# Kernel tuning notes

Hardware: AMD Instinct MI355X
Metric: run time of the kernel (lower is better)

Reference implementation:

```python
import jax, jax.numpy as jnp
import numpy as np

N_NODES = 100000
N_EDGES = 1600000
T = 64          # num_timesteps (graphs)
D_IN = 256
D_H = 256
D_OUT = 16


def setup_inputs() -> dict:
    key = jax.random.key(0)
    ks = jax.random.split(key, 10)
    s = 1.0 / np.sqrt(D_H)
    x = jax.random.normal(ks[0], (N_NODES, D_IN), dtype=jnp.float32)
    edge_index = jax.random.randint(ks[1], (2, N_EDGES), 0, N_NODES, dtype=jnp.int64)
    ptr = (jnp.arange(T + 1, dtype=jnp.int64) * (N_NODES // T))  # even split of nodes into T snapshots
    return {
        "x": x,
        "edge_index": edge_index,
        "ptr": ptr,
        "W1": jax.random.normal(ks[2], (D_IN, D_H), dtype=jnp.float32) * s,
        "b1": jnp.zeros((D_H,), dtype=jnp.float32),
        "W2": jax.random.normal(ks[3], (D_H, D_H), dtype=jnp.float32) * s,
        "b2": jnp.zeros((D_H,), dtype=jnp.float32),
        "w_ih": jax.random.normal(ks[4], (3 * D_H, D_H), dtype=jnp.float32) * s,
        "w_hh": jax.random.normal(ks[5], (3 * D_H, D_H), dtype=jnp.float32) * s,
        "b_ih": jnp.zeros((3 * D_H,), dtype=jnp.float32),
        "b_hh": jnp.zeros((3 * D_H,), dtype=jnp.float32),
        "Wc": jax.random.normal(ks[6], (D_OUT, D_H), dtype=jnp.float32) * s,
        "bc": jnp.zeros((D_OUT,), dtype=jnp.float32),
    }


def _gcn_conv(x, W, b, src, dst, deg_inv_sqrt):
    # PyG GCNConv with self-loops: out_i = sum_j 1/sqrt(d_i d_j) * (x_j W) + (1/d_i) x_i W + b
    xw = x @ W                                            # [N, H]
    coef = deg_inv_sqrt[src] * deg_inv_sqrt[dst]          # [E]
    msg = xw[src] * coef[:, None]                         # [E, H] gather-scale
    agg = jax.ops.segment_sum(msg, dst, num_segments=N_NODES)
    return agg + xw * (deg_inv_sqrt ** 2)[:, None] + b


def _gru_final(seq, w_ih, w_hh, b_ih, b_hh):
    # torch nn.GRU, 1 layer, gate order (r, z, n). seq: [T, H] (batch=1)
    def step(h, x):
        gx = x @ w_ih.T + b_ih
        gh = h @ w_hh.T + b_hh
        xr, xz, xn = jnp.split(gx, 3)
        hr, hz, hn = jnp.split(gh, 3)
        r = jax.nn.sigmoid(xr + hr)
        z = jax.nn.sigmoid(xz + hz)
        n = jnp.tanh(xn + r * hn)
        h_new = (1.0 - z) * n + z * h
        return h_new, None
    h0 = jnp.zeros((D_H,), dtype=seq.dtype)
    h_final, _ = jax.lax.scan(step, h0, seq)
    return h_final


def reference(x, edge_index, ptr, W1, b1, W2, b2, w_ih, w_hh, b_ih, b_hh, Wc, bc):
    src, dst = edge_index[0], edge_index[1]
    # degree with self-loops
    deg = jax.ops.segment_sum(jnp.ones_like(dst, dtype=x.dtype), dst, num_segments=N_NODES) + 1.0
    deg_inv_sqrt = jax.lax.rsqrt(deg)

    h = jax.nn.relu(_gcn_conv(x, W1, b1, src, dst, deg_inv_sqrt))
    h = jax.nn.relu(_gcn_conv(h, W2, b2, src, dst, deg_inv_sqrt))

    # global_mean_pool over timestep segments derived from ptr
    seg = jnp.searchsorted(ptr, jnp.arange(N_NODES), side="right") - 1      # [N]
    sums = jax.ops.segment_sum(h, seg, num_segments=T)                       # [T, H]
    counts = (ptr[1:] - ptr[:-1]).astype(h.dtype)                            # [T]
    h_pooled = sums / jnp.maximum(counts, 1.0)[:, None]

    h_final = _gru_final(h_pooled, w_ih, w_hh, b_ih, b_hh)                   # [H]
    out = h_final @ Wc.T + bc                                                # [D_OUT]
    return out[None, :]                                                     # [1, D_OUT]
```

## Files before the change

kernel.cpp:

```cpp
#include <hip/hip_runtime.h>
#include <hip/hip_bf16.h>
#include <math.h>


static inline size_t align512(size_t x){ return (x + 511) & ~size_t(511); }

typedef _Float16 h2_t __attribute__((ext_vector_type(2)));
typedef unsigned short ushort_t;
typedef short bf16x8 __attribute__((ext_vector_type(8)));
typedef float f32x4 __attribute__((ext_vector_type(4)));
typedef float f32x2 __attribute__((ext_vector_type(2)));

#if defined(__has_builtin)
#if __has_builtin(__builtin_amdgcn_fdot2)
#define HAS_FDOT2 1
#endif
#if __has_builtin(__builtin_amdgcn_cvt_pk_f32_fp8) && __has_builtin(__builtin_amdgcn_cvt_pk_fp8_f32)
#define HAS_FP8CVT 1
#endif
#endif

__device__ inline ushort_t f2bf(float f){
  unsigned u = __float_as_uint(f);
  unsigned r = u + 0x7FFFu + ((u >> 16) & 1u);
  return (ushort_t)(r >> 16);
}
__device__ inline float bf2f(ushort_t h){ return __uint_as_float(((unsigned)h) << 16); }
__device__ inline unsigned pk2bf(float lo, float hi){
  return ((unsigned)f2bf(hi) << 16) | (unsigned)f2bf(lo);
}
__device__ inline bf16x8 as_bf16x8(uint4 u){
  union { uint4 u4; bf16x8 b; } c; c.u4 = u; return c.b;
}


__device__ inline unsigned char f2fp8(float x){
#ifdef HAS_FP8CVT
  int p = __builtin_amdgcn_cvt_pk_fp8_f32(x, x, 0, false);
  return (unsigned char)(p & 0xFF);
#else
  unsigned u = __float_as_uint(x);
  unsigned s = (u >> 24) & 0x80u;
  unsigned um = u & 0x7FFFFFFFu;
  if (um >= 0x43E00000u) return (unsigned char)(s | 0x7E);
  if (um <  0x3C000000u) return (unsigned char)s;
  unsigned r = um + 0x7FFFFu + ((um >> 20) & 1u);
  unsigned e = (r >> 23) & 0xFF, m = (r >> 20) & 7u;
  return (unsigned char)(s | ((e - 120u) << 3) | m);
#endif
}
__device__ inline void fp8x4_to_f32(unsigned v, float& a, float& b, float& c, float& d){
#ifdef HAS_FP8CVT
  f32x2 lo = __builtin_amdgcn_cvt_pk_f32_fp8(v, false);
  f32x2 hi = __builtin_amdgcn_cvt_pk_f32_fp8(v, true);
  a = lo.x; b = lo.y; c = hi.x; d = hi.y;
#else
  auto d1 = [](unsigned char t)->float{
    unsigned s = (t >> 7) & 1u, e = (t >> 3) & 0xFu, m = t & 7u;
    float v = (e == 0) ? ldexpf((float)m, -9) : ldexpf(8.0f + (float)m, (int)e - 10);
    return s ? -v : v;
  };
  a = d1(v & 0xFF); b = d1((v >> 8) & 0xFF); c = d1((v >> 16) & 0xFF); d = d1(v >> 24);
#endif
}


__global__ void count_kernel(const int* __restrict__ ei, int* __restrict__ cnt, int E){
  int e = blockIdx.x*256 + threadIdx.x;
  if (e < E) atomicAdd(&cnt[ei[E + e]], 1);
}

__global__ void dis_kernel(const int* __restrict__ cnt, float* __restrict__ dis, int N){
  int i = blockIdx.x*256 + threadIdx.x;
  if (i < N) dis[i] = rsqrtf((float)cnt[i] + 1.0f);
}

__global__ void scan_block_kernel(const int* __restrict__ cnt, int* __restrict__ rp,
                                  int* __restrict__ bsum, int N){
  __shared__ int s[2][1024];
  int t = threadIdx.x; int i = blockIdx.x*1024 + t;
  int v = (i < N) ? cnt[i] : 0;
  int cur = 0; s[0][t] = v; __syncthreads();
  for (int off = 1; off < 1024; off <<= 1){
    int nxt = cur ^ 1;
    int val = s[cur][t];
    if (t >= off) val += s[cur][t - off];
    s[nxt][t] = val; cur = nxt; __syncthreads();
  }
  if (i < N) rp[i+1] = s[cur][t];
  if (t == 1023) bsum[blockIdx.x] = s[cur][1023];
}

__global__ void scan_sums_kernel(int* __restrict__ bsum, int nb){
  __shared__ int s[128];
  int t = threadIdx.x;
  if (t < nb) s[t] = bsum[t];
  __syncthreads();
  if (t == 0){ int acc = 0; for (int b = 0; b < nb; b++){ int v = s[b]; s[b] = acc; acc += v; } }
  __syncthreads();
  if (t < nb) bsum[t] = s[t];
}

__global__ void add_off_kernel(int* __restrict__ rp, const int* __restrict__ bsum,
                               int* __restrict__ cnt, int N){
  int i = blockIdx.x*256 + threadIdx.x;
  if (i < N){ rp[i+1] += bsum[i >> 10]; cnt[i] = 0; }
  if (i == 0) rp[0] = 0;
}

__global__ void fill_kernel(const int* __restrict__ ei, const int* __restrict__ rp,
                            int* __restrict__ cnt, int* __restrict__ csrc, int E){
  int e = blockIdx.x*256 + threadIdx.x;
  if (e < E){
    int s = ei[e]; int d = ei[E + e];
    int pos = rp[d] + atomicAdd(&cnt[d], 1);
    csrc[pos] = s;
  }
}


__global__ void packW_kernel(const float* __restrict__ W, uint4* __restrict__ Wp){
  int idx = blockIdx.x*256 + threadIdx.x;
  int lane = idx & 63;
  int blk  = idx >> 6;
  int q    = blk & 7;
  int t16  = blk >> 3;
  int n = t16*16 + (lane & 15);
  int k = q*32 + (lane >> 4)*8;
  uint4 v;
  v.x = pk2bf(W[(size_t)(k+0)*256 + n], W[(size_t)(k+1)*256 + n]);
  v.y = pk2bf(W[(size_t)(k+2)*256 + n], W[(size_t)(k+3)*256 + n]);
  v.z = pk2bf(W[(size_t)(k+4)*256 + n], W[(size_t)(k+5)*256 + n]);
  v.w = pk2bf(W[(size_t)(k+6)*256 + n], W[(size_t)(k+7)*256 + n]);
  Wp[idx] = v;
}


template<bool A_BF16>
__global__ __launch_bounds__(256, 2) void gemm_mfma(const void* __restrict__ Ap,
                                                    const uint4* __restrict__ Wp,
                                                    unsigned char* __restrict__ out, int N){
  __shared__ __align__(16) ushort_t As[2][128][40];
  int tid  = threadIdx.x;
  int lane = tid & 63;
  int wave = tid >> 6;
  int wr = wave >> 1, wc = wave & 1;
  int quad = lane >> 4;
  int l15  = lane & 15;
  int r0 = blockIdx.x * 128;
  int cb = blockIdx.y;

  uint4 bfr[4][8];
  {
    const uint4* wpb = Wp + (size_t)(cb*2 + wc) * 2048;
    #pragma unroll
    for (int ct = 0; ct < 4; ct++)
      #pragma unroll
      for (int q = 0; q < 8; q++)
        bfr[ct][q] = wpb[(ct*8 + q)*64 + lane];
  }

  f32x4 acc[4][4];
  #pragma unroll
  for (int rt = 0; rt < 4; rt++)
    #pragma unroll
    for (int ct = 0; ct < 4; ct++)
      acc[rt][ct] = f32x4{0.f, 0.f, 0.f, 0.f};

  int srow = tid >> 1;
  int shalf = tid & 1;
  int grow = min(r0 + srow, N - 1);

  auto load_stage = [&](int it, uint4& v0, uint4& v1){
    int k0 = it*32 + shalf*16;
    if constexpr (A_BF16){
      const ushort_t* Ab = (const ushort_t*)Ap;
      const uint4* ga = (const uint4*)(Ab + (size_t)grow*256 + k0);
      v0 = ga[0]; v1 = ga[1];
    } else {
      const float* Af = (const float*)Ap;
      const float4* ga = (const float4*)(Af + (size_t)grow*256 + k0);
      float4 f0 = ga[0], f1 = ga[1], f2 = ga[2], f3 = ga[3];
      v0.x = pk2bf(f0.x, f0.y); v0.y = pk2bf(f0.z, f0.w);
      v0.z = pk2bf(f1.x, f1.y); v0.w = pk2bf(f1.z, f1.w);
      v1.x = pk2bf(f2.x, f2.y); v1.y = pk2bf(f2.z, f2.w);
      v1.z = pk2bf(f3.x, f3.y); v1.w = pk2bf(f3.z, f3.w);
    }
  };
  auto write_stage = [&](int b, uint4 v0, uint4 v1){
    *(uint4*)&As[b][srow][shalf*16]     = v0;
    *(uint4*)&As[b][srow][shalf*16 + 8] = v1;
  };

  {
    uint4 v0, v1;
    load_stage(0, v0, v1);
    write_stage(0, v0, v1);
  }
  __syncthreads();

  #pragma unroll
  for (int it = 0; it < 8; it++){
    const int b = it & 1;
    uint4 n0, n1;
    if (it < 7) load_stage(it + 1, n0, n1);
    #pragma unroll
    for (int rt = 0; rt < 4; rt++){
      int arow = wr*64 + rt*16 + l15;
      uint4 av = *(const uint4*)&As[b][arow][quad*8];
      bf16x8 af = as_bf16x8(av);
      #pragma unroll
      for (int ct = 0; ct < 4; ct++)
        acc[rt][ct] = __builtin_amdgcn_mfma_f32_16x16x32_bf16(
            af, as_bf16x8(bfr[ct][it]), acc[rt][ct], 0, 0, 0);
    }
    if (it < 7){
      write_stage(b ^ 1, n0, n1);
      __syncthreads();
    }
  }

  int crow0 = r0 + wr*64 + quad*4;
  int ccol0 = cb*128 + wc*64 + l15;
  #pragma unroll
  for (int rt = 0; rt < 4; rt++){
    #pragma unroll
    for (int g = 0; g < 4; g++){
      int row = crow0 + rt*16 + g;
      if (row < N){
        #pragma unroll
        for (int ct = 0; ct < 4; ct++)
          out[(size_t)row*256 + ccol0 + ct*16] = f2fp8(acc[rt][ct][g]);
      }
    }
  }
}


__global__ __launch_bounds__(256) void agg_kernel(const unsigned char* __restrict__ xw,
                                                  const float* __restrict__ dis,
                                                  const int* __restrict__ rp,
                                                  const int* __restrict__ csrc,
                                                  const float* __restrict__ bias,
                                                  ushort_t* __restrict__ out, int N){
  int node = blockIdx.x*8 + (threadIdx.x >> 5);
  int lane = threadIdx.x & 31;
  if (node >= N) return;
  const uint2* xw2 = (const uint2*)xw;
  float di = dis[node];
  float sc = di * di;
  float acc[8];
  {
    uint2 a = xw2[(size_t)node*32 + lane];
    float v0,v1,v2,v3,v4,v5,v6,v7;
    fp8x4_to_f32(a.x, v0, v1, v2, v3);
    fp8x4_to_f32(a.y, v4, v5, v6, v7);
    acc[0]=v0*sc; acc[1]=v1*sc; acc[2]=v2*sc; acc[3]=v3*sc;
    acc[4]=v4*sc; acc[5]=v5*sc; acc[6]=v6*sc; acc[7]=v7*sc;
  }
  int e0 = rp[node], e1 = rp[node+1];
  for (int e = e0; e < e1; e++){
    int s = csrc[e];
    float cc = dis[s] * di;
    uint2 v = xw2[(size_t)s*32 + lane];
    float v0,v1,v2,v3,v4,v5,v6,v7;
    fp8x4_to_f32(v.x, v0, v1, v2, v3);
    fp8x4_to_f32(v.y, v4, v5, v6, v7);
    acc[0] = fmaf(v0, cc, acc[0]);
    acc[1] = fmaf(v1, cc, acc[1]);
    acc[2] = fmaf(v2, cc, acc[2]);
    acc[3] = fmaf(v3, cc, acc[3]);
    acc[4] = fmaf(v4, cc, acc[4]);
    acc[5] = fmaf(v5, cc, acc[5]);
    acc[6] = fmaf(v6, cc, acc[6]);
    acc[7] = fmaf(v7, cc, acc[7]);
  }
  const float4* b4 = (const float4*)bias;
  float4 bA = b4[lane*2], bB = b4[lane*2+1];
  acc[0] = fmaxf(acc[0] + bA.x, 0.f);
  acc[1] = fmaxf(acc[1] + bA.y, 0.f);
  acc[2] = fmaxf(acc[2] + bA.z, 0.f);
  acc[3] = fmaxf(acc[3] + bA.w, 0.f);
  acc[4] = fmaxf(acc[4] + bB.x, 0.f);
  acc[5] = fmaxf(acc[5] + bB.y, 0.f);
  acc[6] = fmaxf(acc[6] + bB.z, 0.f);
  acc[7] = fmaxf(acc[7] + bB.w, 0.f);
  uint4 o;
  o.x = pk2bf(acc[0], acc[1]);
  o.y = pk2bf(acc[2], acc[3]);
  o.z = pk2bf(acc[4], acc[5]);
  o.w = pk2bf(acc[6], acc[7]);
  ((uint4*)out)[(size_t)node*32 + lane] = o;
}


__global__ void pool_kernel(const ushort_t* __restrict__ h, const int* __restrict__ ptr,
                            float* __restrict__ hp){
  int t = blockIdx.x; int part = blockIdx.y; int c = threadIdx.x;
  int s0 = ptr[t], s1 = ptr[t+1];
  int len = s1 - s0;
  int chunk = (len + 7) / 8;
  int r0 = s0 + part*chunk;
  int r1 = min(r0 + chunk, s1);
  float acc = 0.f;
  for (int r = r0; r < r1; r++) acc += bf2f(h[(size_t)r*256 + c]);
  if (r1 > r0) atomicAdd(&hp[t*256 + c], acc);
}

__global__ void hp_div_kernel(float* __restrict__ hp, const int* __restrict__ ptr){
  int t = blockIdx.x; int c = threadIdx.x;
  float cf = (float)max(ptr[t+1] - ptr[t], 1);
  hp[t*256 + c] /= cf;
}


__global__ __launch_bounds__(768) void gx_kernel(const float* __restrict__ hp,
                                                 const float* __restrict__ wih,
                                                 const float* __restrict__ bih,
                                                 float* __restrict__ gx){
  __shared__ float xs[256];
  int t = blockIdx.x; int g = threadIdx.x;
  if (g < 256) xs[g] = hp[t*256 + g];
  __syncthreads();
  float acc = bih[g];
  const float* wr = wih + (size_t)g*256;
  #pragma unroll 4
  for (int k = 0; k < 256; k++) acc = fmaf(xs[k], wr[k], acc);
  gx[t*768 + g] = acc;
}


__global__ __launch_bounds__(512, 2) void gru_kernel(const float* __restrict__ gx,
                                                     const float* __restrict__ whh,
                                                     const float* __restrict__ bhh,
                                                     const float* __restrict__ Wc,
                                                     const float* __restrict__ bc,
                                                     float* __restrict__ out){
  __shared__ _Float16 hh[256];
  __shared__ float hfin[256];
  int tid = threadIdx.x;
  int i = tid >> 1;
  int half = tid & 1;

  h2_t wr[64], wz[64], wn[64];
  {
    const float2* w2 = (const float2*)whh;
    size_t base = (size_t)half * 64;
    const float2* pr = w2 + (size_t)i*128       + base;
    const float2* pz = w2 + (size_t)(i+256)*128 + base;
    const float2* pn = w2 + (size_t)(i+512)*128 + base;
    #pragma unroll
    for (int k = 0; k < 64; k++){
      float2 a = pr[k];
      float2 b = pz[k];
      float2 c = pn[k];
      wr[k] = h2_t{(_Float16)a.x, (_Float16)a.y};
      wz[k] = h2_t{(_Float16)b.x, (_Float16)b.y};
      wn[k] = h2_t{(_Float16)c.x, (_Float16)c.y};
    }
  }
  float bR = bhh[i], bZ = bhh[i+256], bN = bhh[i+512];
  float h = 0.f;

  for (int t = 0; t < 64; t++){
    if (half == 0) hh[i] = (_Float16)h;
    __syncthreads();
    float gxr = gx[t*768 + i];
    float gxz = gx[t*768 + 256 + i];
    float gxn = gx[t*768 + 512 + i];
    const h2_t* hp2 = ((const h2_t*)hh) + half*64;
    float accR = 0.f, accZ = 0.f, accN = 0.f;
    #pragma unroll
    for (int k = 0; k < 64; k++){
      h2_t hv = hp2[k];
#ifdef HAS_FDOT2
      accR = __builtin_amdgcn_fdot2(hv, wr[k], accR, false);
      accZ = __builtin_amdgcn_fdot2(hv, wz[k], accZ, false);
      accN = __builtin_amdgcn_fdot2(hv, wn[k], accN, false);
#else
      accR = fmaf((float)hv.x, (float)wr[k].x, accR);
      accR = fmaf((float)hv.y, (float)wr[k].y, accR);
      accZ = fmaf((float)hv.x, (float)wz[k].x, accZ);
      accZ = fmaf((float)hv.y, (float)wz[k].y, accZ);
      accN = fmaf((float)hv.x, (float)wn[k].x, accN);
      accN = fmaf((float)hv.y, (float)wn[k].y, accN);
#endif
    }
    accR += __shfl_xor(accR, 1);
    accZ += __shfl_xor(accZ, 1);
    accN += __shfl_xor(accN, 1);
    float r = 1.f/(1.f + expf(-(gxr + accR + bR)));
    float z = 1.f/(1.f + expf(-(gxz + accZ + bZ)));
    float n = tanhf(gxn + r*(accN + bN));
    float hnew = (1.f - z)*n + z*h;
    __syncthreads();
    h = hnew;
  }

  if (half == 0) hfin[i] = h;
  __syncthreads();
  if (tid < 16){
    float acc = bc[tid];
    const float* wrow = Wc + (size_t)tid*256;
    for (int k = 0; k < 256; k++) acc = fmaf(hfin[k], wrow[k], acc);
    out[tid] = acc;
  }
}

extern "C" void kernel_launch(void* const* d_in, const int* in_sizes, int n_in,
                              void* d_out, int out_size, void* d_ws, size_t ws_size,
                              hipStream_t stream){
  const float* x   = (const float*)d_in[0];
  const int*   ei  = (const int*)d_in[1];
  const int*   ptr = (const int*)d_in[2];
  const float* W1  = (const float*)d_in[3];
  const float* b1  = (const float*)d_in[4];
  const float* W2  = (const float*)d_in[5];
  const float* b2  = (const float*)d_in[6];
  const float* wih = (const float*)d_in[7];
  const float* whh = (const float*)d_in[8];
  const float* bih = (const float*)d_in[9];
  const float* bhh = (const float*)d_in[10];
  const float* Wc  = (const float*)d_in[11];
  const float* bc  = (const float*)d_in[12];
  float* outp = (float*)d_out;

  const int N = in_sizes[0] / 256;
  const int E = in_sizes[1] / 2;

  char* w = (char*)d_ws;
  size_t off = 0;
  auto alloc = [&](size_t bytes){ void* p = w + off; off = align512(off + bytes); return p; };
  unsigned char* bufA = (unsigned char*)alloc((size_t)N*256);
  ushort_t*      bufB = (ushort_t*)alloc((size_t)N*256*2);
  float* dis  = (float*)alloc((size_t)N*4);
  int*   cnt  = (int*)  alloc((size_t)N*4);
  int*   rp   = (int*)  alloc((size_t)(N+1)*4);
  int*   bsum = (int*)  alloc(128*4);
  int*   csrc = (int*)  alloc((size_t)E*4);
  uint4* Wp1  = (uint4*)alloc(8192*16);
  uint4* Wp2  = (uint4*)alloc(8192*16);
  float* hp   = (float*)alloc((size_t)64*256*4);
  float* gxb  = (float*)alloc((size_t)64*768*4);
  (void)ws_size; (void)n_in; (void)out_size;

  hipMemsetAsync(cnt, 0, (size_t)N*4, stream);
  hipMemsetAsync(hp,  0, (size_t)64*256*4, stream);

  count_kernel<<<(E+255)/256, 256, 0, stream>>>(ei, cnt, E);
  dis_kernel<<<(N+255)/256, 256, 0, stream>>>(cnt, dis, N);
  int nb = (N + 1023) / 1024;
  scan_block_kernel<<<nb, 1024, 0, stream>>>(cnt, rp, bsum, N);
  scan_sums_kernel<<<1, 128, 0, stream>>>(bsum, nb);
  add_off_kernel<<<(N+255)/256, 256, 0, stream>>>(rp, bsum, cnt, N);
  fill_kernel<<<(E+255)/256, 256, 0, stream>>>(ei, rp, cnt, csrc, E);
  packW_kernel<<<32, 256, 0, stream>>>(W1, Wp1);
  packW_kernel<<<32, 256, 0, stream>>>(W2, Wp2);

  gemm_mfma<false><<<dim3((N+127)/128, 2), 256, 0, stream>>>(x, Wp1, bufA, N);
  agg_kernel<<<(N+7)/8, 256, 0, stream>>>(bufA, dis, rp, csrc, b1, bufB, N);
  gemm_mfma<true><<<dim3((N+127)/128, 2), 256, 0, stream>>>(bufB, Wp2, bufA, N);
  agg_kernel<<<(N+7)/8, 256, 0, stream>>>(bufA, dis, rp, csrc, b2, bufB, N);

  pool_kernel<<<dim3(64, 8), 256, 0, stream>>>(bufB, ptr, hp);
  hp_div_kernel<<<64, 256, 0, stream>>>(hp, ptr);
  gx_kernel<<<64, 768, 0, stream>>>(hp, wih, bih, gxb);
  gru_kernel<<<1, 512, 0, stream>>>(gxb, whh, bhh, Wc, bc, outp);
}
```

Baseline: 816.0 us.

## Store GEMM output in column-sliced layout and aggregate per slice with precomputed coefficients

The GEMM now writes its fp8 output as 8 slices of 32 columns, each a contiguous [N,32] array. The aggregation kernel runs one grid dimension per slice, so each slice's gather working set (about 3.2MB) can stay resident in cache instead of gathering full 256-byte rows at random. Edge coefficients dis[s]*dis[d] are computed once in fill_kernel and stored as fp16 in CSR order, which removes the dis[s] gather in both aggregation passes. In exchange, the CSR index and coefficient arrays are read 8 times per pass, there are 8x more threads each doing narrower work, and coefficient precision drops to fp16.

Measured after the change: 1.002 ms. +22.8%, slower.

```diff
diff --git a/kernel.cpp b/kernel.cpp
--- a/kernel.cpp
+++ b/kernel.cpp
@@ -109,12 +109,15 @@
 }
 
 __global__ void fill_kernel(const int* __restrict__ ei, const int* __restrict__ rp,
-                            int* __restrict__ cnt, int* __restrict__ csrc, int E){
+                            int* __restrict__ cnt, int* __restrict__ csrc,
+                            const float* __restrict__ dis, _Float16* __restrict__ coef,
+                            int E){
   int e = blockIdx.x*256 + threadIdx.x;
   if (e < E){
     int s = ei[e]; int d = ei[E + e];
     int pos = rp[d] + atomicAdd(&cnt[d], 1);
     csrc[pos] = s;
+    coef[pos] = (_Float16)(dis[s] * dis[d]);
   }
 }
 
@@ -229,68 +232,59 @@
       int row = crow0 + rt*16 + g;
       if (row < N){
         #pragma unroll
-        for (int ct = 0; ct < 4; ct++)
-          out[(size_t)row*256 + ccol0 + ct*16] = f2fp8(acc[rt][ct][g]);
+        for (int ct = 0; ct < 4; ct++){
+          int col = ccol0 + ct*16;
+          out[((size_t)(col >> 5)*N + row)*32 + (col & 31)] = f2fp8(acc[rt][ct][g]);
+        }
       }
     }
   }
 }
 
 
-__global__ __launch_bounds__(256) void agg_kernel(const unsigned char* __restrict__ xw,
-                                                  const float* __restrict__ dis,
-                                                  const int* __restrict__ rp,
-                                                  const int* __restrict__ csrc,
-                                                  const float* __restrict__ bias,
-                                                  ushort_t* __restrict__ out, int N){
-  int node = blockIdx.x*8 + (threadIdx.x >> 5);
-  int lane = threadIdx.x & 31;
+__global__ __launch_bounds__(256) void agg_slice(const unsigned char* __restrict__ xw,
+                                                 const float* __restrict__ dis,
+                                                 const int* __restrict__ rp,
+                                                 const int* __restrict__ csrc,
+                                                 const _Float16* __restrict__ coef,
+                                                 const float* __restrict__ bias,
+                                                 ushort_t* __restrict__ out, int N){
+  int slice = blockIdx.x;
+  int node  = blockIdx.y*32 + (threadIdx.x >> 3);
+  int lane8 = threadIdx.x & 7;
   if (node >= N) return;
-  const uint2* xw2 = (const uint2*)xw;
+  const unsigned* xwp = (const unsigned*)xw;
+  size_t sbase = (size_t)slice * N;
   float di = dis[node];
-  float sc = di * di;
-  float acc[8];
+  float acc0, acc1, acc2, acc3;
   {
-    uint2 a = xw2[(size_t)node*32 + lane];
-    float v0,v1,v2,v3,v4,v5,v6,v7;
-    fp8x4_to_f32(a.x, v0, v1, v2, v3);
-    fp8x4_to_f32(a.y, v4, v5, v6, v7);
-    acc[0]=v0*sc; acc[1]=v1*sc; acc[2]=v2*sc; acc[3]=v3*sc;
-    acc[4]=v4*sc; acc[5]=v5*sc; acc[6]=v6*sc; acc[7]=v7*sc;
+    unsigned a = xwp[(sbase + node)*8 + lane8];
+    float v0,v1,v2,v3;
+    fp8x4_to_f32(a, v0, v1, v2, v3);
+    float sc = di * di;
+    acc0 = v0*sc; acc1 = v1*sc; acc2 = v2*sc; acc3 = v3*sc;
   }
   int e0 = rp[node], e1 = rp[node+1];
   for (int e = e0; e < e1; e++){
     int s = csrc[e];
-    float cc = dis[s] * di;
-    uint2 v = xw2[(size_t)s*32 + lane];
-    float v0,v1,v2,v3,v4,v5,v6,v7;
-    fp8x4_to_f32(v.x, v0, v1, v2, v3);
-    fp8x4_to_f32(v.y, v4, v5, v6, v7);
-    acc[0] = fmaf(v0, cc, acc[0]);
-    acc[1] = fmaf(v1, cc, acc[1]);
-    acc[2] = fmaf(v2, cc, acc[2]);
-    acc[3] = fmaf(v3, cc, acc[3]);
-    acc[4] = fmaf(v4, cc, acc[4]);
-    acc[5] = fmaf(v5, cc, acc[5]);
-    acc[6] = fmaf(v6, cc, acc[6]);
-    acc[7] = fmaf(v7, cc, acc[7]);
-  }
-  const float4* b4 = (const float4*)bias;
-  float4 bA = b4[lane*2], bB = b4[lane*2+1];
-  acc[0] = fmaxf(acc[0] + bA.x, 0.f);
-  acc[1] = fmaxf(acc[1] + bA.y, 0.f);
-  acc[2] = fmaxf(acc[2] + bA.z, 0.f);
-  acc[3] = fmaxf(acc[3] + bA.w, 0.f);
-  acc[4] = fmaxf(acc[4] + bB.x, 0.f);
-  acc[5] = fmaxf(acc[5] + bB.y, 0.f);
-  acc[6] = fmaxf(acc[6] + bB.z, 0.f);
-  acc[7] = fmaxf(acc[7] + bB.w, 0.f);
-  uint4 o;
-  o.x = pk2bf(acc[0], acc[1]);
-  o.y = pk2bf(acc[2], acc[3]);
-  o.z = pk2bf(acc[4], acc[5]);
-  o.w = pk2bf(acc[6], acc[7]);
-  ((uint4*)out)[(size_t)node*32 + lane] = o;
+    float cc = (float)coef[e];
+    unsigned v = xwp[(sbase + s)*8 + lane8];
+    float v0,v1,v2,v3;
+    fp8x4_to_f32(v, v0, v1, v2, v3);
+    acc0 = fmaf(v0, cc, acc0);
+    acc1 = fmaf(v1, cc, acc1);
+    acc2 = fmaf(v2, cc, acc2);
+    acc3 = fmaf(v3, cc, acc3);
+  }
+  float4 b = ((const float4*)bias)[slice*8 + lane8];
+  acc0 = fmaxf(acc0 + b.x, 0.f);
+  acc1 = fmaxf(acc1 + b.y, 0.f);
+  acc2 = fmaxf(acc2 + b.z, 0.f);
+  acc3 = fmaxf(acc3 + b.w, 0.f);
+  uint2 o;
+  o.x = pk2bf(acc0, acc1);
+  o.y = pk2bf(acc2, acc3);
+  ((uint2*)out)[(size_t)node*64 + slice*8 + lane8] = o;
 }
 
 
@@ -438,6 +432,7 @@
   int*   rp   = (int*)  alloc((size_t)(N+1)*4);
   int*   bsum = (int*)  alloc(128*4);
   int*   csrc = (int*)  alloc((size_t)E*4);
+  _Float16* coef = (_Float16*)alloc((size_t)E*2);
   uint4* Wp1  = (uint4*)alloc(8192*16);
   uint4* Wp2  = (uint4*)alloc(8192*16);
   float* hp   = (float*)alloc((size_t)64*256*4);
@@ -453,14 +448,14 @@
   scan_block_kernel<<<nb, 1024, 0, stream>>>(cnt, rp, bsum, N);
   scan_sums_kernel<<<1, 128, 0, stream>>>(bsum, nb);
   add_off_kernel<<<(N+255)/256, 256, 0, stream>>>(rp, bsum, cnt, N);
-  fill_kernel<<<(E+255)/256, 256, 0, stream>>>(ei, rp, cnt, csrc, E);
+  fill_kernel<<<(E+255)/256, 256, 0, stream>>>(ei, rp, cnt, csrc, dis, coef, E);
   packW_kernel<<<32, 256, 0, stream>>>(W1, Wp1);
   packW_kernel<<<32, 256, 0, stream>>>(W2, Wp2);
 
   gemm_mfma<false><<<dim3((N+127)/128, 2), 256, 0, stream>>>(x, Wp1, bufA, N);
-  agg_kernel<<<(N+7)/8, 256, 0, stream>>>(bufA, dis, rp, csrc, b1, bufB, N);
+  agg_slice<<<dim3(8, (N+31)/32), 256, 0, stream>>>(bufA, dis, rp, csrc, coef, b1, bufB, N);
   gemm_mfma<true><<<dim3((N+127)/128, 2), 256, 0, stream>>>(bufB, Wp2, bufA, N);
-  agg_kernel<<<(N+7)/8, 256, 0, stream>>>(bufA, dis, rp, csrc, b2, bufB, N);
+  agg_slice<<<dim3(8, (N+31)/32), 256, 0, stream>>>(bufA, dis, rp, csrc, coef, b2, bufB, N);
 
   pool_kernel<<<dim3(64, 8), 256, 0, stream>>>(bufB, ptr, hp);
   hp_div_kernel<<<64, 256, 0, stream>>>(hp, ptr);
```
